# Kernel tuning notes

Hardware: AMD Instinct MI355X
Metric: run time of the kernel (lower is better)

Reference implementation:

```python
import jax, jax.numpy as jnp
import numpy as np

B, C, H = 16, 512, 32
HID, NB, S, P, SR = 512, 36, 26, 7, 2
SCALE = 32.0
N_LOC, N_LOC_LAB = 12, 8
N_GRP, GRP_SZ, N_GRP_LAB = 4, 6, 16
IN_DIM = P * P * C


def roi_align(feat, coords, scale, pooled, sr):
    # feat: (B,C,H,W); coords: (B,NB,4) normalized xyxy. torchvision roi_align,
    # aligned=False, fixed sampling_ratio=sr (adaptive ratio is data-dependent).
    Bs, Cc, Hh, Ww = feat.shape
    x1 = coords[..., 0] * scale
    y1 = coords[..., 1] * scale
    x2 = coords[..., 2] * scale
    y2 = coords[..., 3] * scale
    rw = jnp.maximum(x2 - x1, 1.0)
    rh = jnp.maximum(y2 - y1, 1.0)
    bw = rw / pooled
    bh = rh / pooled
    # sample offsets within roi, in bin units: (pooled*sr,)
    off = (jnp.arange(pooled)[:, None] + (jnp.arange(sr) + 0.5) / sr).reshape(-1)
    ys = y1[..., None] + off * bh[..., None]  # (B,NB,pooled*sr)
    xs = x1[..., None] + off * bw[..., None]

    def prep(t, size):
        valid = (t > -1.0) & (t < size)
        tc = jnp.clip(t, 0.0, size - 1)
        lo = jnp.floor(tc).astype(jnp.int32)
        hi = jnp.minimum(lo + 1, size - 1)
        frac = tc - lo
        return lo, hi, frac, valid

    y_lo, y_hi, ly, vy = prep(ys, Hh)
    x_lo, x_hi, lx, vx = prep(xs, Ww)
    hy, hx = 1.0 - ly, 1.0 - lx

    featl = feat.transpose(0, 2, 3, 1)  # (B,H,W,C)
    b_idx = jnp.arange(Bs)[:, None, None, None]

    def gather(yi, xi):
        # -> (B,NB,Py,Px,C)
        return featl[b_idx, yi[:, :, :, None], xi[:, :, None, :]]

    def w(a, b):
        return (a[..., :, None] * b[..., None, :])[..., None]

    val = (gather(y_lo, x_lo) * w(hy, hx) + gather(y_lo, x_hi) * w(hy, lx)
           + gather(y_hi, x_lo) * w(ly, hx) + gather(y_hi, x_hi) * w(ly, lx))
    mask = (vy[:, :, :, None] & vx[:, :, None, :])[..., None]
    val = jnp.where(mask, val, 0.0)
    val = val.reshape(Bs, -1, pooled, sr, pooled, sr, Cc).mean(axis=(3, 5))
    return val.transpose(0, 1, 4, 2, 3)  # (B,NB,C,pooled,pooled)


def setup_inputs() -> dict:
    key = jax.random.key(0)
    ks = jax.random.split(key, 10)
    lf = jax.random.normal(ks[0], (B, C, H, H), dtype=jnp.float32)
    xs = jnp.sort(jax.random.uniform(ks[1], (B, S, 2)), axis=-1)
    ys = jnp.sort(jax.random.uniform(ks[2], (B, S, 2)), axis=-1)
    coords = jnp.stack([xs[..., 0], ys[..., 0], xs[..., 1], ys[..., 1]], axis=-1)
    sc = 0.02
    return {
        'local_features': lf,
        'pred_bbox_coords': coords,
        'roi_fc_W': jax.random.normal(ks[3], (HID, IN_DIM), dtype=jnp.float32) * sc,
        'roi_fc_b': jnp.zeros((HID,), jnp.float32),
        'coords_W': jax.random.normal(ks[4], (S, 4, HID), dtype=jnp.float32) * sc,
        'coords_b': jnp.zeros((S, 4), jnp.float32),
        'pres_W': jax.random.normal(ks[5], (S, HID), dtype=jnp.float32) * sc,
        'pres_b': jnp.zeros((S,), jnp.float32),
        'loc_W': jax.random.normal(ks[6], (N_LOC, N_LOC_LAB, HID), dtype=jnp.float32) * sc,
        'loc_b': jnp.zeros((N_LOC, N_LOC_LAB), jnp.float32),
        'grp_W': jax.random.normal(ks[7], (N_GRP, N_GRP_LAB, GRP_SZ * HID), dtype=jnp.float32) * sc,
        'grp_b': jnp.zeros((N_GRP, N_GRP_LAB), jnp.float32),
        'loc_idx': jnp.arange(N_LOC, dtype=jnp.int32),
        'grp_idx': jnp.arange(N_GRP * GRP_SZ, dtype=jnp.int32).reshape(N_GRP, GRP_SZ),
    }


def reference(local_features, pred_bbox_coords, roi_fc_W, roi_fc_b, coords_W,
              coords_b, pres_W, pres_b, loc_W, loc_b, grp_W, grp_b, loc_idx, grp_idx):
    Bs = local_features.shape[0]
    # boxes S..NB default to the full image (0,0,1,1)
    full = jnp.broadcast_to(jnp.array([0.0, 0.0, 1.0, 1.0], jnp.float32), (Bs, NB, 4))
    coords_all = full.at[:, :S].set(pred_bbox_coords)
    roi = roi_align(local_features, coords_all, SCALE, P, SR)  # (B,NB,C,P,P)
    flat = roi.reshape(Bs, NB, IN_DIM)
    feats = jax.nn.relu(jnp.einsum('bnf,hf->bnh', flat, roi_fc_W) + roi_fc_b)
    sup = feats[:, :S]  # (B,S,HID)
    # per-box coord refinement heads
    deltas = jnp.einsum('bsh,soh->bso', sup, coords_W) + coords_b  # (B,S,4)
    w = pred_bbox_coords[..., 2] - pred_bbox_coords[..., 0]
    h = pred_bbox_coords[..., 3] - pred_bbox_coords[..., 1]
    wh = jnp.stack([w, h, w, h], axis=-1)
    refined = pred_bbox_coords + deltas * wh
    presence = jnp.einsum('bsh,sh->bs', sup, pres_W) + pres_b  # (B,S)
    # per-box MLC heads
    loc = jnp.einsum('blh,loh->blo', feats[:, loc_idx], loc_W) + loc_b
    # per-group MLC heads (concat box feats within group along hidden)
    gf = feats[:, grp_idx].reshape(Bs, N_GRP, GRP_SZ * HID)
    grp = jnp.einsum('bgk,gok->bgo', gf, grp_W) + grp_b
    mlc = jnp.concatenate([loc.reshape(Bs, -1), grp.reshape(Bs, -1)], axis=1)
    return refined, presence, mlc
```

## Files before the change

kernel.cpp:

```cpp
#include <hip/hip_runtime.h>

typedef unsigned short u16;
typedef __attribute__((ext_vector_type(8))) short short8;
typedef __attribute__((ext_vector_type(8))) unsigned short ushort8_t;
typedef __attribute__((ext_vector_type(4))) float f32x4;
typedef __attribute__((ext_vector_type(2))) float v2f;

#define BATCH   16
#define CCH     512
#define NBOX    36
#define SS      26
#define INDIM   25088
#define HIDN    512
#define M_ROWS  416
#define KSPLIT  56
#define KITERS  7
#define NKB     392

__device__ __forceinline__ u16 f2bf(float f) {
  unsigned u = __float_as_uint(f);
  u += 0x7FFF + ((u >> 16) & 1);
  return (u16)(u >> 16);
}
__device__ __forceinline__ float bf2f(u16 h) {
  return __uint_as_float(((unsigned)h) << 16);
}
__device__ __forceinline__ v2f bf2x2(u16 a, u16 b) {
  v2f r;
  r.x = __uint_as_float(((unsigned)a) << 16);
  r.y = __uint_as_float(((unsigned)b) << 16);
  return r;
}

__global__ __launch_bounds__(256) void k_transpose_lf(const float* __restrict__ in,
                                                      u16* __restrict__ out) {
  __shared__ u16 t[32][66];
  int b = blockIdx.z, y = blockIdx.y, ct = blockIdx.x;
  int tid = threadIdx.x;

  int cl = tid >> 2;
  int xq = (tid & 3) * 8;
  const float* src = in + ((size_t)(b * CCH + ct * 64 + cl) * 1024) + y * 32 + xq;
  float4 v0 = *(const float4*)src;
  float4 v1 = *(const float4*)(src + 4);
  t[xq + 0][cl] = f2bf(v0.x); t[xq + 1][cl] = f2bf(v0.y);
  t[xq + 2][cl] = f2bf(v0.z); t[xq + 3][cl] = f2bf(v0.w);
  t[xq + 4][cl] = f2bf(v1.x); t[xq + 5][cl] = f2bf(v1.y);
  t[xq + 6][cl] = f2bf(v1.z); t[xq + 7][cl] = f2bf(v1.w);
  __syncthreads();

  int xl = tid >> 3;
  int cq = (tid & 7) * 8;
  ushort8_t o;
#pragma unroll
  for (int i = 0; i < 8; ++i) o[i] = t[xl][cq + i];
  *(ushort8_t*)(out + ((size_t)b * 1024 + y * 32 + xl) * CCH + ct * 64 + cq) = o;
}

#define WPAD 532
__global__ __launch_bounds__(256) void k_convert_w(const float* __restrict__ in,
                                                   u16* __restrict__ out) {
  __shared__ u16 s[49 * WPAD];
  int h = blockIdx.x;
  int tid = threadIdx.x;
  const float4* src = (const float4*)(in + (size_t)h * INDIM);
  for (int i = tid; i < 6272; i += 256) {
    float4 v = src[i];
    int k = i * 4;
#pragma unroll
    for (int j = 0; j < 4; ++j) {
      int kk = k + j;
      int c = kk / 49;
      int p = kk - c * 49;
      s[p * WPAD + c] = f2bf((&v.x)[j]);
    }
  }
  __syncthreads();
  for (int q = tid; q < 3136; q += 256) {
    int p = q >> 6;
    int c0 = (q & 63) * 8;
    const u16* sp = &s[p * WPAD + c0];
    ushort8_t o;
#pragma unroll
    for (int i = 0; i < 8; ++i) o[i] = sp[i];
    int kb = p * 8 + (c0 >> 6);
    int col = c0 & 63;
    *(ushort8_t*)(out + ((size_t)kb * HIDN + h) * 64 + col) = o;
  }
}

__global__ __launch_bounds__(512) void k_roi(const u16* __restrict__ lf_t,
                                             const float* __restrict__ pred,
                                             u16* __restrict__ flat2) {
  __shared__ int   s_ylo[14], s_yhi[14], s_xlo[14], s_xhi[14];
  __shared__ float s_wyl[14], s_wyh[14], s_wxl[14], s_wxh[14];

  int bid = blockIdx.x;
  int xcd = bid & 7;
  int s = bid >> 3;
  int b = xcd * 2 + (s >= 26 ? 1 : 0);
  int n = (s >= 26) ? s - 26 : s;
  int blk = b * 26 + n;
  int t = threadIdx.x;

  if (t < 28) {
    bool isY = t < 14;
    int j = isY ? t : t - 14;
    const float* p = pred + ((size_t)(b * SS + n)) * 4;
    float c0 = p[0], c1 = p[1], c2 = p[2], c3 = p[3];
    float lo1 = (isY ? c1 : c0) * 32.f;
    float hi1 = (isY ? c3 : c2) * 32.f;
    float sz = fmaxf(hi1 - lo1, 1.f);
    float bs = sz * (1.f / 7.f);
    float off = (float)(j >> 1) + 0.25f + 0.5f * (float)(j & 1);
    float pos = lo1 + off * bs;
    bool valid = (pos > -1.f) && (pos < 32.f);
    float tc = fminf(fmaxf(pos, 0.f), 31.f);
    int lo = (int)floorf(tc);
    int hi = min(lo + 1, 31);
    float fr = tc - (float)lo;
    float wl = valid ? (1.f - fr) : 0.f;
    float wh = valid ? fr : 0.f;
    if (isY) { s_ylo[j] = lo; s_yhi[j] = hi; s_wyl[j] = wl; s_wyh[j] = wh; }
    else     { s_xlo[j] = lo; s_xhi[j] = hi; s_wxl[j] = wl; s_wxh[j] = wh; }
  }
  __syncthreads();

  int cg = t & 63;
  int pg = t >> 6;
  const u16* base = lf_t + (size_t)b * 1024 * CCH + cg * 8;

  for (int p = pg; p < 49; p += 8) {
    int py = p / 7, px = p % 7;
    v2f a0 = {0.f, 0.f}, a1 = {0.f, 0.f}, a2 = {0.f, 0.f}, a3 = {0.f, 0.f};
#pragma unroll
    for (int sy = 0; sy < 2; ++sy) {
      int jy = 2 * py + sy;
      const u16* rlo = base + s_ylo[jy] * 32 * CCH;
      const u16* rhi = base + s_yhi[jy] * 32 * CCH;
      float wyl = s_wyl[jy], wyh = s_wyh[jy];
#pragma unroll
      for (int sx = 0; sx < 2; ++sx) {
        int jx = 2 * px + sx;
        int xl = s_xlo[jx] * CCH, xh = s_xhi[jx] * CCH;
        v2f wll = {wyl * s_wxl[jx], wyl * s_wxl[jx]};
        v2f wlh = {wyl * s_wxh[jx], wyl * s_wxh[jx]};
        v2f whl = {wyh * s_wxl[jx], wyh * s_wxl[jx]};
        v2f whh = {wyh * s_wxh[jx], wyh * s_wxh[jx]};
        ushort8_t vll = *(const ushort8_t*)(rlo + xl);
        ushort8_t vlh = *(const ushort8_t*)(rlo + xh);
        ushort8_t vhl = *(const ushort8_t*)(rhi + xl);
        ushort8_t vhh = *(const ushort8_t*)(rhi + xh);
        a0 += wll * bf2x2(vll[0], vll[1]) + wlh * bf2x2(vlh[0], vlh[1])
            + whl * bf2x2(vhl[0], vhl[1]) + whh * bf2x2(vhh[0], vhh[1]);
        a1 += wll * bf2x2(vll[2], vll[3]) + wlh * bf2x2(vlh[2], vlh[3])
            + whl * bf2x2(vhl[2], vhl[3]) + whh * bf2x2(vhh[2], vhh[3]);
        a2 += wll * bf2x2(vll[4], vll[5]) + wlh * bf2x2(vlh[4], vlh[5])
            + whl * bf2x2(vhl[4], vhl[5]) + whh * bf2x2(vhh[4], vhh[5]);
        a3 += wll * bf2x2(vll[6], vll[7]) + wlh * bf2x2(vlh[6], vlh[7])
            + whl * bf2x2(vhl[6], vhl[7]) + whh * bf2x2(vhh[6], vhh[7]);
      }
    }
    ushort8_t o;
    o[0] = f2bf(a0.x * 0.25f); o[1] = f2bf(a0.y * 0.25f);
    o[2] = f2bf(a1.x * 0.25f); o[3] = f2bf(a1.y * 0.25f);
    o[4] = f2bf(a2.x * 0.25f); o[5] = f2bf(a2.y * 0.25f);
    o[6] = f2bf(a3.x * 0.25f); o[7] = f2bf(a3.y * 0.25f);
    int kb = p * 8 + (cg >> 3);
    int col = (cg & 7) * 8;
    *(ushort8_t*)(flat2 + ((size_t)kb * M_ROWS + blk) * 64 + col) = o;
  }
}

__global__ __launch_bounds__(256) void k_gemm(const u16* __restrict__ flat2,
                                              const u16* __restrict__ Wb2,
                                              u16* __restrict__ partials) {
  __shared__ u16 As[128 * 64];
  __shared__ u16 Bs[128 * 64];

  int tid = threadIdx.x;
  int wave = tid >> 6, lane = tid & 63;
  int wm = wave >> 1, wn = wave & 1;
  int quad = lane >> 4, r = lane & 15;
  int xb = r & 7;

  int bid = blockIdx.x;
  int xcd = bid & 7;
  int slot = bid >> 3;
  int z = xcd * 7 + (slot >> 4);
  int xy = slot & 15;
  int tileN0 = (xy & 3) * 128;
  int tileM0 = (xy >> 2) * 128;
  int kb0 = z * KITERS;

  size_t aoff[4], boff[4];
  int    ldso[4];
#pragma unroll
  for (int t = 0; t < 4; ++t) {
    int chunk = (wave * 4 + t) * 64 + lane;
    int row = chunk >> 3;
    int lc = chunk & 7;
    ldso[t] = row * 64 + ((lc ^ (row & 7)) << 3);
    int grow = min(tileM0 + row, M_ROWS - 1);
    aoff[t] = ((size_t)kb0 * M_ROWS + grow) * 64 + lc * 8;
    boff[t] = ((size_t)kb0 * HIDN + tileN0 + row) * 64 + lc * 8;
  }

  f32x4 acc[4][4];
#pragma unroll
  for (int mi = 0; mi < 4; ++mi)
#pragma unroll
    for (int ni = 0; ni < 4; ++ni) acc[mi][ni] = (f32x4){0.f, 0.f, 0.f, 0.f};

  short8 ra[4], rb[4];
#pragma unroll
  for (int t = 0; t < 4; ++t) {
    ra[t] = *(const short8*)(flat2 + aoff[t]);
    rb[t] = *(const short8*)(Wb2 + boff[t]);
  }

  for (int kt = 0; kt < KITERS; ++kt) {
#pragma unroll
    for (int t = 0; t < 4; ++t) {
      *(short8*)&As[ldso[t]] = ra[t];
      *(short8*)&Bs[ldso[t]] = rb[t];
    }
    __syncthreads();

    if (kt + 1 < KITERS) {
      size_t ak = (size_t)(kt + 1) * (M_ROWS * 64);
      size_t bk = (size_t)(kt + 1) * (HIDN * 64);
#pragma unroll
      for (int t = 0; t < 4; ++t) {
        ra[t] = *(const short8*)(flat2 + aoff[t] + ak);
        rb[t] = *(const short8*)(Wb2 + boff[t] + bk);
      }
    }

#pragma unroll
    for (int kk = 0; kk < 64; kk += 32) {
      int k8 = kk >> 3;
      int pc = ((k8 + quad) ^ xb) << 3;
      short8 af[4], bfr[4];
#pragma unroll
      for (int mi = 0; mi < 4; ++mi)
        af[mi] = *(const short8*)&As[(wm * 64 + mi * 16 + r) * 64 + pc];
#pragma unroll
      for (int ni = 0; ni < 4; ++ni)
        bfr[ni] = *(const short8*)&Bs[(wn * 64 + ni * 16 + r) * 64 + pc];
#pragma unroll
      for (int mi = 0; mi < 4; ++mi)
#pragma unroll
        for (int ni = 0; ni < 4; ++ni)
          acc[mi][ni] = __builtin_amdgcn_mfma_f32_16x16x32_bf16(
              af[mi], bfr[ni], acc[mi][ni], 0, 0, 0);
    }
    __syncthreads();
  }

  u16* part = partials + (size_t)z * (M_ROWS * HIDN);
#pragma unroll
  for (int mi = 0; mi < 4; ++mi)
#pragma unroll
    for (int ni = 0; ni < 4; ++ni) {
      int row0 = tileM0 + wm * 64 + mi * 16 + quad * 4;
      int col = tileN0 + wn * 64 + ni * 16 + r;
#pragma unroll
      for (int reg = 0; reg < 4; ++reg) {
        int row = row0 + reg;
        if (row < M_ROWS) part[(size_t)row * HIDN + col] = f2bf(acc[mi][ni][reg]);
      }
    }
}

__global__ __launch_bounds__(256) void k_reduce(const u16* __restrict__ partials,
                                                const float* __restrict__ bias,
                                                float* __restrict__ feats) {
  int gid = blockIdx.x * 256 + threadIdx.x;
  int row = gid >> 6;
  int c0 = (gid & 63) * 8;
  float s[8] = {0.f, 0.f, 0.f, 0.f, 0.f, 0.f, 0.f, 0.f};
  const u16* p = partials + (size_t)row * HIDN + c0;
  for (int z = 0; z < KSPLIT; ++z) {
    ushort8_t v = *(const ushort8_t*)(p + (size_t)z * (M_ROWS * HIDN));
#pragma unroll
    for (int j = 0; j < 8; ++j) s[j] += bf2f(v[j]);
  }
  float4 o0, o1;
  const float* bi = bias + c0;
  o0.x = fmaxf(s[0] + bi[0], 0.f); o0.y = fmaxf(s[1] + bi[1], 0.f);
  o0.z = fmaxf(s[2] + bi[2], 0.f); o0.w = fmaxf(s[3] + bi[3], 0.f);
  o1.x = fmaxf(s[4] + bi[4], 0.f); o1.y = fmaxf(s[5] + bi[5], 0.f);
  o1.z = fmaxf(s[6] + bi[6], 0.f); o1.w = fmaxf(s[7] + bi[7], 0.f);
  float* dst = feats + (size_t)row * HIDN + c0;
  *(float4*)dst = o0;
  *(float4*)(dst + 4) = o1;
}

__device__ __forceinline__ float wave_red(float s) {
#pragma unroll
  for (int off = 32; off > 0; off >>= 1) s += __shfl_down(s, off);
  return s;
}

__device__ __forceinline__ float dot512(const float* __restrict__ f,
                                        const float* __restrict__ w, int lane) {
  const float4* f4 = (const float4*)f;
  const float4* w4 = (const float4*)w;
  float4 x0 = f4[lane], y0 = w4[lane];
  float4 x1 = f4[lane + 64], y1 = w4[lane + 64];
  return x0.x * y0.x + x0.y * y0.y + x0.z * y0.z + x0.w * y0.w +
         x1.x * y1.x + x1.y * y1.y + x1.z * y1.z + x1.w * y1.w;
}

__global__ __launch_bounds__(256) void k_heads(const float* __restrict__ feats,
                                               const float* __restrict__ pred,
                                               const float* __restrict__ cW,
                                               const float* __restrict__ cb,
                                               const float* __restrict__ pW,
                                               const float* __restrict__ pb,
                                               const float* __restrict__ lW,
                                               const float* __restrict__ lb,
                                               const float* __restrict__ gW,
                                               const float* __restrict__ gb,
                                               const int* __restrict__ lidx,
                                               const int* __restrict__ gidx,
                                               float* __restrict__ out) {
  int wid = blockIdx.x * 4 + (threadIdx.x >> 6);
  int lane = threadIdx.x & 63;
  float sum = 0.f;

  if (wid < 1664) {
    int b = wid / 104, rr = wid % 104, s = rr >> 2, o = rr & 3;
    sum = dot512(feats + (size_t)(b * 26 + s) * HIDN,
                 cW + (size_t)(s * 4 + o) * HIDN, lane);
    sum = wave_red(sum);
    if (lane == 0) {
      const float* p = pred + (size_t)(b * SS + s) * 4;
      float wdt = p[2] - p[0], hgt = p[3] - p[1];
      float whv = (o & 1) ? hgt : wdt;
      out[wid] = p[o] + (sum + cb[s * 4 + o]) * whv;
    }
  } else if (wid < 2080) {
    int i = wid - 1664;
    int b = i / 26, s = i % 26;
    sum = dot512(feats + (size_t)(b * 26 + s) * HIDN,
                 pW + (size_t)s * HIDN, lane);
    sum = wave_red(sum);
    if (lane == 0) out[1664 + i] = sum + pb[s];
  } else if (wid < 3616) {
    int i = wid - 2080;
    int b = i / 96, rr = i % 96, l = rr >> 3, o = rr & 7;
    sum = dot512(feats + (size_t)(b * 26 + lidx[l]) * HIDN,
                 lW + (size_t)(l * 8 + o) * HIDN, lane);
    sum = wave_red(sum);
    if (lane == 0) out[2080 + b * 160 + rr] = sum + lb[l * 8 + o];
  } else {
    int i = wid - 3616;
    int b = i / 64, rr = i % 64, g = rr >> 4, o = rr & 15;
    const float* w = gW + (size_t)(g * 16 + o) * 3072;
#pragma unroll
    for (int jj = 0; jj < 6; ++jj) {
      sum += dot512(feats + (size_t)(b * 26 + gidx[g * 6 + jj]) * HIDN,
                    w + jj * 512, lane);
    }
    sum = wave_red(sum);
    if (lane == 0) out[2080 + b * 160 + 96 + rr] = sum + gb[g * 16 + o];
  }
}

extern "C" void kernel_launch(void* const* d_in, const int* in_sizes, int n_in,
                              void* d_out, int out_size, void* d_ws, size_t ws_size,
                              hipStream_t stream) {
  const float* lf      = (const float*)d_in[0];
  const float* pred    = (const float*)d_in[1];
  const float* roiW    = (const float*)d_in[2];
  const float* roiB    = (const float*)d_in[3];
  const float* cW      = (const float*)d_in[4];
  const float* cb      = (const float*)d_in[5];
  const float* pW      = (const float*)d_in[6];
  const float* pb      = (const float*)d_in[7];
  const float* lW      = (const float*)d_in[8];
  const float* lb      = (const float*)d_in[9];
  const float* gW      = (const float*)d_in[10];
  const float* gb      = (const float*)d_in[11];
  const int*   lidx    = (const int*)d_in[12];
  const int*   gidx    = (const int*)d_in[13];
  float* out = (float*)d_out;

  char* ws = (char*)d_ws;
  u16*   lf_t     = (u16*)ws;
  u16*   partials = (u16*)ws;
  u16*   Wb2   = (u16*)(ws + 33030144);
  u16*   flat2 = (u16*)(ws + 33030144 + 25690112);
  float* feats = (float*)(ws + 33030144 + 25690112 + 28901376);

  k_transpose_lf<<<dim3(8, 32, 16), 256, 0, stream>>>(lf, lf_t);
  k_convert_w<<<HIDN, 256, 0, stream>>>(roiW, Wb2);
  k_roi<<<M_ROWS, 512, 0, stream>>>(lf_t, pred, flat2);
  k_gemm<<<896, 256, 0, stream>>>(flat2, Wb2, partials);
  k_reduce<<<(M_ROWS * HIDN / 8) / 256, 256, 0, stream>>>(partials, roiB, feats);
  k_heads<<<1160, 256, 0, stream>>>(feats, pred, cW, cb, pW, pb, lW, lb, gW, gb,
                                    lidx, gidx, out);
}
```

Measured before the change: 203.2 us.

## Fuse all stages into one persistent kernel with software grid barriers

Merges the transpose, weight conversion, ROI align, split-K GEMM, reduction and head kernels into one persistent kernel of 256 blocks. The stages are separated by atomic-counter grid barriers, and a memset resets the counter before launch. This removes five kernel launches and the idle gaps between them. In exchange, several stages run on fewer blocks than before (256 instead of up to 4096), the barriers add spin-wait cost, and correctness relies on all 256 blocks being resident at once.

```diff
diff --git a/kernel.cpp b/kernel.cpp
--- a/kernel.cpp
+++ b/kernel.cpp
@@ -16,6 +16,7 @@
 #define KSPLIT  56
 #define KITERS  7
 #define NKB     392
+#define GRID    256
 
 __device__ __forceinline__ u16 f2bf(float f) {
   unsigned u = __float_as_uint(f);
@@ -32,269 +33,45 @@
   return r;
 }
 
-__global__ __launch_bounds__(256) void k_transpose_lf(const float* __restrict__ in,
-                                                      u16* __restrict__ out) {
-  __shared__ u16 t[32][66];
-  int b = blockIdx.z, y = blockIdx.y, ct = blockIdx.x;
-  int tid = threadIdx.x;
-
-  int cl = tid >> 2;
-  int xq = (tid & 3) * 8;
-  const float* src = in + ((size_t)(b * CCH + ct * 64 + cl) * 1024) + y * 32 + xq;
-  float4 v0 = *(const float4*)src;
-  float4 v1 = *(const float4*)(src + 4);
-  t[xq + 0][cl] = f2bf(v0.x); t[xq + 1][cl] = f2bf(v0.y);
-  t[xq + 2][cl] = f2bf(v0.z); t[xq + 3][cl] = f2bf(v0.w);
-  t[xq + 4][cl] = f2bf(v1.x); t[xq + 5][cl] = f2bf(v1.y);
-  t[xq + 6][cl] = f2bf(v1.z); t[xq + 7][cl] = f2bf(v1.w);
+struct KParams {
+  const float* lf;
+  const float* pred;
+  const float* roiW;
+  const float* roiB;
+  const float* cW;  const float* cb;
+  const float* pW;  const float* pb;
+  const float* lW;  const float* lb;
+  const float* gW;  const float* gb;
+  const int* lidx;  const int* gidx;
+  float* out;
+  u16* lf_t;
+  u16* Wb2;
+  u16* flat2;
+  u16* partials;
+  float* feats;
+  unsigned* bar;
+};
+
+union SMem {
+  u16 tr[32][66];
+  u16 cv[49 * 132];
+  struct { u16 A[128 * 64]; u16 B[128 * 64]; } g;
+  struct {
+    int   ylo[14], yhi[14], xlo[14], xhi[14];
+    float wyl[14], wyh[14], wxl[14], wxh[14];
+  } roi;
+};
+
+__device__ __forceinline__ void gbar(unsigned* ctr, unsigned target, int t) {
   __syncthreads();
-
-  int xl = tid >> 3;
-  int cq = (tid & 7) * 8;
-  ushort8_t o;
-#pragma unroll
-  for (int i = 0; i < 8; ++i) o[i] = t[xl][cq + i];
-  *(ushort8_t*)(out + ((size_t)b * 1024 + y * 32 + xl) * CCH + ct * 64 + cq) = o;
-}
-
-#define WPAD 532
-__global__ __launch_bounds__(256) void k_convert_w(const float* __restrict__ in,
-                                                   u16* __restrict__ out) {
-  __shared__ u16 s[49 * WPAD];
-  int h = blockIdx.x;
-  int tid = threadIdx.x;
-  const float4* src = (const float4*)(in + (size_t)h * INDIM);
-  for (int i = tid; i < 6272; i += 256) {
-    float4 v = src[i];
-    int k = i * 4;
-#pragma unroll
-    for (int j = 0; j < 4; ++j) {
-      int kk = k + j;
-      int c = kk / 49;
-      int p = kk - c * 49;
-      s[p * WPAD + c] = f2bf((&v.x)[j]);
-    }
+  if (t == 0) {
+    __threadfence();
+    __hip_atomic_fetch_add(ctr, 1u, __ATOMIC_ACQ_REL, __HIP_MEMORY_SCOPE_AGENT);
+    while (__hip_atomic_load(ctr, __ATOMIC_ACQUIRE, __HIP_MEMORY_SCOPE_AGENT) < target)
+      __builtin_amdgcn_s_sleep(2);
+    __threadfence();
   }
   __syncthreads();
-  for (int q = tid; q < 3136; q += 256) {
-    int p = q >> 6;
-    int c0 = (q & 63) * 8;
-    const u16* sp = &s[p * WPAD + c0];
-    ushort8_t o;
-#pragma unroll
-    for (int i = 0; i < 8; ++i) o[i] = sp[i];
-    int kb = p * 8 + (c0 >> 6);
-    int col = c0 & 63;
-    *(ushort8_t*)(out + ((size_t)kb * HIDN + h) * 64 + col) = o;
-  }
-}
-
-__global__ __launch_bounds__(512) void k_roi(const u16* __restrict__ lf_t,
-                                             const float* __restrict__ pred,
-                                             u16* __restrict__ flat2) {
-  __shared__ int   s_ylo[14], s_yhi[14], s_xlo[14], s_xhi[14];
-  __shared__ float s_wyl[14], s_wyh[14], s_wxl[14], s_wxh[14];
-
-  int bid = blockIdx.x;
-  int xcd = bid & 7;
-  int s = bid >> 3;
-  int b = xcd * 2 + (s >= 26 ? 1 : 0);
-  int n = (s >= 26) ? s - 26 : s;
-  int blk = b * 26 + n;
-  int t = threadIdx.x;
-
-  if (t < 28) {
-    bool isY = t < 14;
-    int j = isY ? t : t - 14;
-    const float* p = pred + ((size_t)(b * SS + n)) * 4;
-    float c0 = p[0], c1 = p[1], c2 = p[2], c3 = p[3];
-    float lo1 = (isY ? c1 : c0) * 32.f;
-    float hi1 = (isY ? c3 : c2) * 32.f;
-    float sz = fmaxf(hi1 - lo1, 1.f);
-    float bs = sz * (1.f / 7.f);
-    float off = (float)(j >> 1) + 0.25f + 0.5f * (float)(j & 1);
-    float pos = lo1 + off * bs;
-    bool valid = (pos > -1.f) && (pos < 32.f);
-    float tc = fminf(fmaxf(pos, 0.f), 31.f);
-    int lo = (int)floorf(tc);
-    int hi = min(lo + 1, 31);
-    float fr = tc - (float)lo;
-    float wl = valid ? (1.f - fr) : 0.f;
-    float wh = valid ? fr : 0.f;
-    if (isY) { s_ylo[j] = lo; s_yhi[j] = hi; s_wyl[j] = wl; s_wyh[j] = wh; }
-    else     { s_xlo[j] = lo; s_xhi[j] = hi; s_wxl[j] = wl; s_wxh[j] = wh; }
-  }
-  __syncthreads();
-
-  int cg = t & 63;
-  int pg = t >> 6;
-  const u16* base = lf_t + (size_t)b * 1024 * CCH + cg * 8;
-
-  for (int p = pg; p < 49; p += 8) {
-    int py = p / 7, px = p % 7;
-    v2f a0 = {0.f, 0.f}, a1 = {0.f, 0.f}, a2 = {0.f, 0.f}, a3 = {0.f, 0.f};
-#pragma unroll
-    for (int sy = 0; sy < 2; ++sy) {
-      int jy = 2 * py + sy;
-      const u16* rlo = base + s_ylo[jy] * 32 * CCH;
-      const u16* rhi = base + s_yhi[jy] * 32 * CCH;
-      float wyl = s_wyl[jy], wyh = s_wyh[jy];
-#pragma unroll
-      for (int sx = 0; sx < 2; ++sx) {
-        int jx = 2 * px + sx;
-        int xl = s_xlo[jx] * CCH, xh = s_xhi[jx] * CCH;
-        v2f wll = {wyl * s_wxl[jx], wyl * s_wxl[jx]};
-        v2f wlh = {wyl * s_wxh[jx], wyl * s_wxh[jx]};
-        v2f whl = {wyh * s_wxl[jx], wyh * s_wxl[jx]};
-        v2f whh = {wyh * s_wxh[jx], wyh * s_wxh[jx]};
-        ushort8_t vll = *(const ushort8_t*)(rlo + xl);
-        ushort8_t vlh = *(const ushort8_t*)(rlo + xh);
-        ushort8_t vhl = *(const ushort8_t*)(rhi + xl);
-        ushort8_t vhh = *(const ushort8_t*)(rhi + xh);
-        a0 += wll * bf2x2(vll[0], vll[1]) + wlh * bf2x2(vlh[0], vlh[1])
-            + whl * bf2x2(vhl[0], vhl[1]) + whh * bf2x2(vhh[0], vhh[1]);
-        a1 += wll * bf2x2(vll[2], vll[3]) + wlh * bf2x2(vlh[2], vlh[3])
-            + whl * bf2x2(vhl[2], vhl[3]) + whh * bf2x2(vhh[2], vhh[3]);
-        a2 += wll * bf2x2(vll[4], vll[5]) + wlh * bf2x2(vlh[4], vlh[5])
-            + whl * bf2x2(vhl[4], vhl[5]) + whh * bf2x2(vhh[4], vhh[5]);
-        a3 += wll * bf2x2(vll[6], vll[7]) + wlh * bf2x2(vlh[6], vlh[7])
-            + whl * bf2x2(vhl[6], vhl[7]) + whh * bf2x2(vhh[6], vhh[7]);
-      }
-    }
-    ushort8_t o;
-    o[0] = f2bf(a0.x * 0.25f); o[1] = f2bf(a0.y * 0.25f);
-    o[2] = f2bf(a1.x * 0.25f); o[3] = f2bf(a1.y * 0.25f);
-    o[4] = f2bf(a2.x * 0.25f); o[5] = f2bf(a2.y * 0.25f);
-    o[6] = f2bf(a3.x * 0.25f); o[7] = f2bf(a3.y * 0.25f);
-    int kb = p * 8 + (cg >> 3);
-    int col = (cg & 7) * 8;
-    *(ushort8_t*)(flat2 + ((size_t)kb * M_ROWS + blk) * 64 + col) = o;
-  }
-}
-
-__global__ __launch_bounds__(256) void k_gemm(const u16* __restrict__ flat2,
-                                              const u16* __restrict__ Wb2,
-                                              u16* __restrict__ partials) {
-  __shared__ u16 As[128 * 64];
-  __shared__ u16 Bs[128 * 64];
-
-  int tid = threadIdx.x;
-  int wave = tid >> 6, lane = tid & 63;
-  int wm = wave >> 1, wn = wave & 1;
-  int quad = lane >> 4, r = lane & 15;
-  int xb = r & 7;
-
-  int bid = blockIdx.x;
-  int xcd = bid & 7;
-  int slot = bid >> 3;
-  int z = xcd * 7 + (slot >> 4);
-  int xy = slot & 15;
-  int tileN0 = (xy & 3) * 128;
-  int tileM0 = (xy >> 2) * 128;
-  int kb0 = z * KITERS;
-
-  size_t aoff[4], boff[4];
-  int    ldso[4];
-#pragma unroll
-  for (int t = 0; t < 4; ++t) {
-    int chunk = (wave * 4 + t) * 64 + lane;
-    int row = chunk >> 3;
-    int lc = chunk & 7;
-    ldso[t] = row * 64 + ((lc ^ (row & 7)) << 3);
-    int grow = min(tileM0 + row, M_ROWS - 1);
-    aoff[t] = ((size_t)kb0 * M_ROWS + grow) * 64 + lc * 8;
-    boff[t] = ((size_t)kb0 * HIDN + tileN0 + row) * 64 + lc * 8;
-  }
-
-  f32x4 acc[4][4];
-#pragma unroll
-  for (int mi = 0; mi < 4; ++mi)
-#pragma unroll
-    for (int ni = 0; ni < 4; ++ni) acc[mi][ni] = (f32x4){0.f, 0.f, 0.f, 0.f};
-
-  short8 ra[4], rb[4];
-#pragma unroll
-  for (int t = 0; t < 4; ++t) {
-    ra[t] = *(const short8*)(flat2 + aoff[t]);
-    rb[t] = *(const short8*)(Wb2 + boff[t]);
-  }
-
-  for (int kt = 0; kt < KITERS; ++kt) {
-#pragma unroll
-    for (int t = 0; t < 4; ++t) {
-      *(short8*)&As[ldso[t]] = ra[t];
-      *(short8*)&Bs[ldso[t]] = rb[t];
-    }
-    __syncthreads();
-
-    if (kt + 1 < KITERS) {
-      size_t ak = (size_t)(kt + 1) * (M_ROWS * 64);
-      size_t bk = (size_t)(kt + 1) * (HIDN * 64);
-#pragma unroll
-      for (int t = 0; t < 4; ++t) {
-        ra[t] = *(const short8*)(flat2 + aoff[t] + ak);
-        rb[t] = *(const short8*)(Wb2 + boff[t] + bk);
-      }
-    }
-
-#pragma unroll
-    for (int kk = 0; kk < 64; kk += 32) {
-      int k8 = kk >> 3;
-      int pc = ((k8 + quad) ^ xb) << 3;
-      short8 af[4], bfr[4];
-#pragma unroll
-      for (int mi = 0; mi < 4; ++mi)
-        af[mi] = *(const short8*)&As[(wm * 64 + mi * 16 + r) * 64 + pc];
-#pragma unroll
-      for (int ni = 0; ni < 4; ++ni)
-        bfr[ni] = *(const short8*)&Bs[(wn * 64 + ni * 16 + r) * 64 + pc];
-#pragma unroll
-      for (int mi = 0; mi < 4; ++mi)
-#pragma unroll
-        for (int ni = 0; ni < 4; ++ni)
-          acc[mi][ni] = __builtin_amdgcn_mfma_f32_16x16x32_bf16(
-              af[mi], bfr[ni], acc[mi][ni], 0, 0, 0);
-    }
-    __syncthreads();
-  }
-
-  u16* part = partials + (size_t)z * (M_ROWS * HIDN);
-#pragma unroll
-  for (int mi = 0; mi < 4; ++mi)
-#pragma unroll
-    for (int ni = 0; ni < 4; ++ni) {
-      int row0 = tileM0 + wm * 64 + mi * 16 + quad * 4;
-      int col = tileN0 + wn * 64 + ni * 16 + r;
-#pragma unroll
-      for (int reg = 0; reg < 4; ++reg) {
-        int row = row0 + reg;
-        if (row < M_ROWS) part[(size_t)row * HIDN + col] = f2bf(acc[mi][ni][reg]);
-      }
-    }
-}
-
-__global__ __launch_bounds__(256) void k_reduce(const u16* __restrict__ partials,
-                                                const float* __restrict__ bias,
-                                                float* __restrict__ feats) {
-  int gid = blockIdx.x * 256 + threadIdx.x;
-  int row = gid >> 6;
-  int c0 = (gid & 63) * 8;
-  float s[8] = {0.f, 0.f, 0.f, 0.f, 0.f, 0.f, 0.f, 0.f};
-  const u16* p = partials + (size_t)row * HIDN + c0;
-  for (int z = 0; z < KSPLIT; ++z) {
-    ushort8_t v = *(const ushort8_t*)(p + (size_t)z * (M_ROWS * HIDN));
-#pragma unroll
-    for (int j = 0; j < 8; ++j) s[j] += bf2f(v[j]);
-  }
-  float4 o0, o1;
-  const float* bi = bias + c0;
-  o0.x = fmaxf(s[0] + bi[0], 0.f); o0.y = fmaxf(s[1] + bi[1], 0.f);
-  o0.z = fmaxf(s[2] + bi[2], 0.f); o0.w = fmaxf(s[3] + bi[3], 0.f);
-  o1.x = fmaxf(s[4] + bi[4], 0.f); o1.y = fmaxf(s[5] + bi[5], 0.f);
-  o1.z = fmaxf(s[6] + bi[6], 0.f); o1.w = fmaxf(s[7] + bi[7], 0.f);
-  float* dst = feats + (size_t)row * HIDN + c0;
-  *(float4*)dst = o0;
-  *(float4*)(dst + 4) = o1;
 }
 
 __device__ __forceinline__ float wave_red(float s) {
@@ -313,93 +90,337 @@
          x1.x * y1.x + x1.y * y1.y + x1.z * y1.z + x1.w * y1.w;
 }
 
-__global__ __launch_bounds__(256) void k_heads(const float* __restrict__ feats,
-                                               const float* __restrict__ pred,
-                                               const float* __restrict__ cW,
-                                               const float* __restrict__ cb,
-                                               const float* __restrict__ pW,
-                                               const float* __restrict__ pb,
-                                               const float* __restrict__ lW,
-                                               const float* __restrict__ lb,
-                                               const float* __restrict__ gW,
-                                               const float* __restrict__ gb,
-                                               const int* __restrict__ lidx,
-                                               const int* __restrict__ gidx,
-                                               float* __restrict__ out) {
-  int wid = blockIdx.x * 4 + (threadIdx.x >> 6);
-  int lane = threadIdx.x & 63;
-  float sum = 0.f;
-
-  if (wid < 1664) {
-    int b = wid / 104, rr = wid % 104, s = rr >> 2, o = rr & 3;
-    sum = dot512(feats + (size_t)(b * 26 + s) * HIDN,
-                 cW + (size_t)(s * 4 + o) * HIDN, lane);
-    sum = wave_red(sum);
-    if (lane == 0) {
-      const float* p = pred + (size_t)(b * SS + s) * 4;
-      float wdt = p[2] - p[0], hgt = p[3] - p[1];
-      float whv = (o & 1) ? hgt : wdt;
-      out[wid] = p[o] + (sum + cb[s * 4 + o]) * whv;
-    }
-  } else if (wid < 2080) {
-    int i = wid - 1664;
-    int b = i / 26, s = i % 26;
-    sum = dot512(feats + (size_t)(b * 26 + s) * HIDN,
-                 pW + (size_t)s * HIDN, lane);
-    sum = wave_red(sum);
-    if (lane == 0) out[1664 + i] = sum + pb[s];
-  } else if (wid < 3616) {
-    int i = wid - 2080;
-    int b = i / 96, rr = i % 96, l = rr >> 3, o = rr & 7;
-    sum = dot512(feats + (size_t)(b * 26 + lidx[l]) * HIDN,
-                 lW + (size_t)(l * 8 + o) * HIDN, lane);
-    sum = wave_red(sum);
-    if (lane == 0) out[2080 + b * 160 + rr] = sum + lb[l * 8 + o];
-  } else {
-    int i = wid - 3616;
-    int b = i / 64, rr = i % 64, g = rr >> 4, o = rr & 15;
-    const float* w = gW + (size_t)(g * 16 + o) * 3072;
-#pragma unroll
-    for (int jj = 0; jj < 6; ++jj) {
-      sum += dot512(feats + (size_t)(b * 26 + gidx[g * 6 + jj]) * HIDN,
-                    w + jj * 512, lane);
-    }
-    sum = wave_red(sum);
-    if (lane == 0) out[2080 + b * 160 + 96 + rr] = sum + gb[g * 16 + o];
+__global__ __launch_bounds__(256, 2) void k_fused(KParams P) {
+  __shared__ SMem sm;
+  const int t   = threadIdx.x;
+  const int bid = blockIdx.x;
+
+  for (int j = bid; j < 6144; j += GRID) {
+    if (j < 4096) {
+      int ct = j & 7, y = (j >> 3) & 31, b = j >> 8;
+      int cl = t >> 2;
+      int xq = (t & 3) * 8;
+      const float* src = P.lf + ((size_t)(b * CCH + ct * 64 + cl) * 1024) + y * 32 + xq;
+      float4 v0 = *(const float4*)src;
+      float4 v1 = *(const float4*)(src + 4);
+      sm.tr[xq + 0][cl] = f2bf(v0.x); sm.tr[xq + 1][cl] = f2bf(v0.y);
+      sm.tr[xq + 2][cl] = f2bf(v0.z); sm.tr[xq + 3][cl] = f2bf(v0.w);
+      sm.tr[xq + 4][cl] = f2bf(v1.x); sm.tr[xq + 5][cl] = f2bf(v1.y);
+      sm.tr[xq + 6][cl] = f2bf(v1.z); sm.tr[xq + 7][cl] = f2bf(v1.w);
+      __syncthreads();
+      int xl = t >> 3;
+      int cq = (t & 7) * 8;
+      ushort8_t o;
+#pragma unroll
+      for (int i = 0; i < 8; ++i) o[i] = sm.tr[xl][cq + i];
+      *(ushort8_t*)(P.lf_t + ((size_t)b * 1024 + y * 32 + xl) * CCH + ct * 64 + cq) = o;
+    } else {
+      int j2 = j - 4096;
+      int h  = j2 >> 2;
+      int c0 = (j2 & 3) * 128;
+      const float4* s4 = (const float4*)(P.roiW + (size_t)h * INDIM + (size_t)c0 * 49);
+      for (int i = t; i < 1568; i += 256) {
+        float4 v = s4[i];
+        int k = i * 4;
+#pragma unroll
+        for (int jj = 0; jj < 4; ++jj) {
+          int kk = k + jj;
+          int cc = kk / 49;
+          int p  = kk - cc * 49;
+          sm.cv[p * 132 + cc] = f2bf((&v.x)[jj]);
+        }
+      }
+      __syncthreads();
+      for (int q = t; q < 784; q += 256) {
+        int p = q >> 4;
+        int cc0 = (q & 15) * 8;
+        const u16* sp = &sm.cv[p * 132 + cc0];
+        ushort8_t o;
+#pragma unroll
+        for (int i = 0; i < 8; ++i) o[i] = sp[i];
+        int c   = c0 + cc0;
+        int kb  = p * 8 + (c >> 6);
+        int col = c & 63;
+        *(ushort8_t*)(P.Wb2 + ((size_t)kb * HIDN + h) * 64 + col) = o;
+      }
+    }
+    __syncthreads();
+  }
+  gbar(P.bar, 1 * GRID, t);
+
+  for (int j = bid; j < 832; j += GRID) {
+    int half = (j >= 416) ? 1 : 0;
+    int bj   = half ? j - 416 : j;
+    int xcd  = bj & 7;
+    int s    = bj >> 3;
+    int b    = xcd * 2 + (s >= 26 ? 1 : 0);
+    int n    = (s >= 26) ? s - 26 : s;
+    int blk  = b * 26 + n;
+
+    if (t < 28) {
+      bool isY = t < 14;
+      int jj = isY ? t : t - 14;
+      const float* pp = P.pred + ((size_t)(b * SS + n)) * 4;
+      float c0 = pp[0], c1 = pp[1], c2 = pp[2], c3 = pp[3];
+      float lo1 = (isY ? c1 : c0) * 32.f;
+      float hi1 = (isY ? c3 : c2) * 32.f;
+      float sz = fmaxf(hi1 - lo1, 1.f);
+      float bs = sz * (1.f / 7.f);
+      float off = (float)(jj >> 1) + 0.25f + 0.5f * (float)(jj & 1);
+      float pos = lo1 + off * bs;
+      bool valid = (pos > -1.f) && (pos < 32.f);
+      float tc = fminf(fmaxf(pos, 0.f), 31.f);
+      int lo = (int)floorf(tc);
+      int hi = min(lo + 1, 31);
+      float fr = tc - (float)lo;
+      float wl = valid ? (1.f - fr) : 0.f;
+      float wh = valid ? fr : 0.f;
+      if (isY) { sm.roi.ylo[jj] = lo; sm.roi.yhi[jj] = hi;
+                 sm.roi.wyl[jj] = wl; sm.roi.wyh[jj] = wh; }
+      else     { sm.roi.xlo[jj] = lo; sm.roi.xhi[jj] = hi;
+                 sm.roi.wxl[jj] = wl; sm.roi.wxh[jj] = wh; }
+    }
+    __syncthreads();
+
+    int cgi = t & 63;
+    int pg  = t >> 6;
+    const u16* base = P.lf_t + (size_t)b * 1024 * CCH + cgi * 8;
+    int pend = half ? 49 : 24;
+
+    for (int p = (half ? 24 : 0) + pg; p < pend; p += 4) {
+      int py = p / 7, px = p % 7;
+      v2f a0 = {0.f, 0.f}, a1 = {0.f, 0.f}, a2 = {0.f, 0.f}, a3 = {0.f, 0.f};
+#pragma unroll
+      for (int sy = 0; sy < 2; ++sy) {
+        int jy = 2 * py + sy;
+        const u16* rlo = base + sm.roi.ylo[jy] * 32 * CCH;
+        const u16* rhi = base + sm.roi.yhi[jy] * 32 * CCH;
+        float wyl = sm.roi.wyl[jy], wyh = sm.roi.wyh[jy];
+#pragma unroll
+        for (int sx = 0; sx < 2; ++sx) {
+          int jx = 2 * px + sx;
+          int xl = sm.roi.xlo[jx] * CCH, xh = sm.roi.xhi[jx] * CCH;
+          v2f wll = {wyl * sm.roi.wxl[jx], wyl * sm.roi.wxl[jx]};
+          v2f wlh = {wyl * sm.roi.wxh[jx], wyl * sm.roi.wxh[jx]};
+          v2f whl = {wyh * sm.roi.wxl[jx], wyh * sm.roi.wxl[jx]};
+          v2f whh = {wyh * sm.roi.wxh[jx], wyh * sm.roi.wxh[jx]};
+          ushort8_t vll = *(const ushort8_t*)(rlo + xl);
+          ushort8_t vlh = *(const ushort8_t*)(rlo + xh);
+          ushort8_t vhl = *(const ushort8_t*)(rhi + xl);
+          ushort8_t vhh = *(const ushort8_t*)(rhi + xh);
+          a0 += wll * bf2x2(vll[0], vll[1]) + wlh * bf2x2(vlh[0], vlh[1])
+              + whl * bf2x2(vhl[0], vhl[1]) + whh * bf2x2(vhh[0], vhh[1]);
+          a1 += wll * bf2x2(vll[2], vll[3]) + wlh * bf2x2(vlh[2], vlh[3])
+              + whl * bf2x2(vhl[2], vhl[3]) + whh * bf2x2(vhh[2], vhh[3]);
+          a2 += wll * bf2x2(vll[4], vll[5]) + wlh * bf2x2(vlh[4], vlh[5])
+              + whl * bf2x2(vhl[4], vhl[5]) + whh * bf2x2(vhh[4], vhh[5]);
+          a3 += wll * bf2x2(vll[6], vll[7]) + wlh * bf2x2(vlh[6], vlh[7])
+              + whl * bf2x2(vhl[6], vhl[7]) + whh * bf2x2(vhh[6], vhh[7]);
+        }
+      }
+      ushort8_t o;
+      o[0] = f2bf(a0.x * 0.25f); o[1] = f2bf(a0.y * 0.25f);
+      o[2] = f2bf(a1.x * 0.25f); o[3] = f2bf(a1.y * 0.25f);
+      o[4] = f2bf(a2.x * 0.25f); o[5] = f2bf(a2.y * 0.25f);
+      o[6] = f2bf(a3.x * 0.25f); o[7] = f2bf(a3.y * 0.25f);
+      int kb  = p * 8 + (cgi >> 3);
+      int col = (cgi & 7) * 8;
+      *(ushort8_t*)(P.flat2 + ((size_t)kb * M_ROWS + blk) * 64 + col) = o;
+    }
+    __syncthreads();
+  }
+  gbar(P.bar, 2 * GRID, t);
+
+  for (int job = bid; job < 896; job += GRID) {
+    int wave = t >> 6, lane = t & 63;
+    int wm = wave >> 1, wn = wave & 1;
+    int quad = lane >> 4, r = lane & 15;
+    int xb = r & 7;
+
+    int xcd2 = job & 7;
+    int slot = job >> 3;
+    int z  = xcd2 * 7 + (slot >> 4);
+    int xy = slot & 15;
+    int tileN0 = (xy & 3) * 128;
+    int tileM0 = (xy >> 2) * 128;
+    int kb0 = z * KITERS;
+
+    size_t aoff[4], boff[4];
+    int    ldso[4];
+#pragma unroll
+    for (int tt = 0; tt < 4; ++tt) {
+      int chunk = (wave * 4 + tt) * 64 + lane;
+      int row = chunk >> 3;
+      int lc  = chunk & 7;
+      ldso[tt] = row * 64 + ((lc ^ (row & 7)) << 3);
+      int grow = min(tileM0 + row, M_ROWS - 1);
+      aoff[tt] = ((size_t)kb0 * M_ROWS + grow) * 64 + lc * 8;
+      boff[tt] = ((size_t)kb0 * HIDN + tileN0 + row) * 64 + lc * 8;
+    }
+
+    f32x4 acc[4][4];
+#pragma unroll
+    for (int mi = 0; mi < 4; ++mi)
+#pragma unroll
+      for (int ni = 0; ni < 4; ++ni) acc[mi][ni] = (f32x4){0.f, 0.f, 0.f, 0.f};
+
+    short8 ra[4], rb[4];
+#pragma unroll
+    for (int tt = 0; tt < 4; ++tt) {
+      ra[tt] = *(const short8*)(P.flat2 + aoff[tt]);
+      rb[tt] = *(const short8*)(P.Wb2 + boff[tt]);
+    }
+
+    for (int kt = 0; kt < KITERS; ++kt) {
+#pragma unroll
+      for (int tt = 0; tt < 4; ++tt) {
+        *(short8*)&sm.g.A[ldso[tt]] = ra[tt];
+        *(short8*)&sm.g.B[ldso[tt]] = rb[tt];
+      }
+      __syncthreads();
+
+      if (kt + 1 < KITERS) {
+        size_t ak = (size_t)(kt + 1) * (M_ROWS * 64);
+        size_t bk = (size_t)(kt + 1) * (HIDN * 64);
+#pragma unroll
+        for (int tt = 0; tt < 4; ++tt) {
+          ra[tt] = *(const short8*)(P.flat2 + aoff[tt] + ak);
+          rb[tt] = *(const short8*)(P.Wb2 + boff[tt] + bk);
+        }
+      }
+
+#pragma unroll
+      for (int kk = 0; kk < 64; kk += 32) {
+        int k8 = kk >> 3;
+        int pc = ((k8 + quad) ^ xb) << 3;
+        short8 af[4], bfr[4];
+#pragma unroll
+        for (int mi = 0; mi < 4; ++mi)
+          af[mi] = *(const short8*)&sm.g.A[(wm * 64 + mi * 16 + r) * 64 + pc];
+#pragma unroll
+        for (int ni = 0; ni < 4; ++ni)
+          bfr[ni] = *(const short8*)&sm.g.B[(wn * 64 + ni * 16 + r) * 64 + pc];
+#pragma unroll
+        for (int mi = 0; mi < 4; ++mi)
+#pragma unroll
+          for (int ni = 0; ni < 4; ++ni)
+            acc[mi][ni] = __builtin_amdgcn_mfma_f32_16x16x32_bf16(
+                af[mi], bfr[ni], acc[mi][ni], 0, 0, 0);
+      }
+      __syncthreads();
+    }
+
+    u16* part = P.partials + (size_t)z * (M_ROWS * HIDN);
+#pragma unroll
+    for (int mi = 0; mi < 4; ++mi)
+#pragma unroll
+      for (int ni = 0; ni < 4; ++ni) {
+        int row0 = tileM0 + wm * 64 + mi * 16 + quad * 4;
+        int col  = tileN0 + wn * 64 + ni * 16 + r;
+#pragma unroll
+        for (int reg = 0; reg < 4; ++reg) {
+          int row = row0 + reg;
+          if (row < M_ROWS) part[(size_t)row * HIDN + col] = f2bf(acc[mi][ni][reg]);
+        }
+      }
+  }
+  gbar(P.bar, 3 * GRID, t);
+
+  for (int gid = bid * 256 + t; gid < M_ROWS * HIDN / 8; gid += GRID * 256) {
+    int row = gid >> 6;
+    int c0  = (gid & 63) * 8;
+    float s[8] = {0.f, 0.f, 0.f, 0.f, 0.f, 0.f, 0.f, 0.f};
+    const u16* p = P.partials + (size_t)row * HIDN + c0;
+    for (int z = 0; z < KSPLIT; ++z) {
+      ushort8_t v = *(const ushort8_t*)(p + (size_t)z * (M_ROWS * HIDN));
+#pragma unroll
+      for (int jj = 0; jj < 8; ++jj) s[jj] += bf2f(v[jj]);
+    }
+    float4 o0, o1;
+    const float* bi = P.roiB + c0;
+    o0.x = fmaxf(s[0] + bi[0], 0.f); o0.y = fmaxf(s[1] + bi[1], 0.f);
+    o0.z = fmaxf(s[2] + bi[2], 0.f); o0.w = fmaxf(s[3] + bi[3], 0.f);
+    o1.x = fmaxf(s[4] + bi[4], 0.f); o1.y = fmaxf(s[5] + bi[5], 0.f);
+    o1.z = fmaxf(s[6] + bi[6], 0.f); o1.w = fmaxf(s[7] + bi[7], 0.f);
+    float* dst = P.feats + (size_t)row * HIDN + c0;
+    *(float4*)dst = o0;
+    *(float4*)(dst + 4) = o1;
+  }
+  gbar(P.bar, 4 * GRID, t);
+
+  for (int j = bid; j < 1160; j += GRID) {
+    int wid  = j * 4 + (t >> 6);
+    int lane = t & 63;
+    float sum = 0.f;
+
+    if (wid < 1664) {
+      int b = wid / 104, rr = wid % 104, s = rr >> 2, o = rr & 3;
+      sum = dot512(P.feats + (size_t)(b * 26 + s) * HIDN,
+                   P.cW + (size_t)(s * 4 + o) * HIDN, lane);
+      sum = wave_red(sum);
+      if (lane == 0) {
+        const float* pp = P.pred + (size_t)(b * SS + s) * 4;
+        float wdt = pp[2] - pp[0], hgt = pp[3] - pp[1];
+        float whv = (o & 1) ? hgt : wdt;
+        P.out[wid] = pp[o] + (sum + P.cb[s * 4 + o]) * whv;
+      }
+    } else if (wid < 2080) {
+      int i = wid - 1664;
+      int b = i / 26, s = i % 26;
+      sum = dot512(P.feats + (size_t)(b * 26 + s) * HIDN,
+                   P.pW + (size_t)s * HIDN, lane);
+      sum = wave_red(sum);
+      if (lane == 0) P.out[1664 + i] = sum + P.pb[s];
+    } else if (wid < 3616) {
+      int i = wid - 2080;
+      int b = i / 96, rr = i % 96, l = rr >> 3, o = rr & 7;
+      sum = dot512(P.feats + (size_t)(b * 26 + P.lidx[l]) * HIDN,
+                   P.lW + (size_t)(l * 8 + o) * HIDN, lane);
+      sum = wave_red(sum);
+      if (lane == 0) P.out[2080 + b * 160 + rr] = sum + P.lb[l * 8 + o];
+    } else {
+      int i = wid - 3616;
+      int b = i / 64, rr = i % 64, g = rr >> 4, o = rr & 15;
+      const float* w = P.gW + (size_t)(g * 16 + o) * 3072;
+#pragma unroll
+      for (int jj = 0; jj < 6; ++jj) {
+        sum += dot512(P.feats + (size_t)(b * 26 + P.gidx[g * 6 + jj]) * HIDN,
+                      w + jj * 512, lane);
+      }
+      sum = wave_red(sum);
+      if (lane == 0) P.out[2080 + b * 160 + 96 + rr] = sum + P.gb[g * 16 + o];
+    }
   }
 }
 
 extern "C" void kernel_launch(void* const* d_in, const int* in_sizes, int n_in,
                               void* d_out, int out_size, void* d_ws, size_t ws_size,
                               hipStream_t stream) {
-  const float* lf      = (const float*)d_in[0];
-  const float* pred    = (const float*)d_in[1];
-  const float* roiW    = (const float*)d_in[2];
-  const float* roiB    = (const float*)d_in[3];
-  const float* cW      = (const float*)d_in[4];
-  const float* cb      = (const float*)d_in[5];
-  const float* pW      = (const float*)d_in[6];
-  const float* pb      = (const float*)d_in[7];
-  const float* lW      = (const float*)d_in[8];
-  const float* lb      = (const float*)d_in[9];
-  const float* gW      = (const float*)d_in[10];
-  const float* gb      = (const float*)d_in[11];
-  const int*   lidx    = (const int*)d_in[12];
-  const int*   gidx    = (const int*)d_in[13];
-  float* out = (float*)d_out;
-
   char* ws = (char*)d_ws;
-  u16*   lf_t     = (u16*)ws;
-  u16*   partials = (u16*)ws;
-  u16*   Wb2   = (u16*)(ws + 33030144);
-  u16*   flat2 = (u16*)(ws + 33030144 + 25690112);
-  float* feats = (float*)(ws + 33030144 + 25690112 + 28901376);
-
-  k_transpose_lf<<<dim3(8, 32, 16), 256, 0, stream>>>(lf, lf_t);
-  k_convert_w<<<HIDN, 256, 0, stream>>>(roiW, Wb2);
-  k_roi<<<M_ROWS, 512, 0, stream>>>(lf_t, pred, flat2);
-  k_gemm<<<896, 256, 0, stream>>>(flat2, Wb2, partials);
-  k_reduce<<<(M_ROWS * HIDN / 8) / 256, 256, 0, stream>>>(partials, roiB, feats);
-  k_heads<<<1160, 256, 0, stream>>>(feats, pred, cW, cb, pW, pb, lW, lb, gW, gb,
-                                    lidx, gidx, out);
-}
+
+  KParams hp;
+  hp.lf    = (const float*)d_in[0];
+  hp.pred  = (const float*)d_in[1];
+  hp.roiW  = (const float*)d_in[2];
+  hp.roiB  = (const float*)d_in[3];
+  hp.cW    = (const float*)d_in[4];
+  hp.cb    = (const float*)d_in[5];
+  hp.pW    = (const float*)d_in[6];
+  hp.pb    = (const float*)d_in[7];
+  hp.lW    = (const float*)d_in[8];
+  hp.lb    = (const float*)d_in[9];
+  hp.gW    = (const float*)d_in[10];
+  hp.gb    = (const float*)d_in[11];
+  hp.lidx  = (const int*)d_in[12];
+  hp.gidx  = (const int*)d_in[13];
+  hp.out   = (float*)d_out;
+  hp.lf_t     = (u16*)ws;
+  hp.partials = (u16*)ws;
+  hp.Wb2      = (u16*)(ws + 33030144);
+  hp.flat2    = (u16*)(ws + 33030144 + 25690112);
+  hp.bar      = (unsigned*)(ws + 33030144 + 25690112 + 20873216);
+  hp.feats    = (float*)(ws + 33030144 + 25690112 + 28901376);
+
+  hipMemsetAsync((void*)hp.bar, 0, 64, stream);
+  k_fused<<<dim3(GRID), dim3(256), 0, stream>>>(hp);
+}
```

Measured after the change: 434.7 us. 114% more time.

## Merge preprocessing kernels and split weight conversion and reduction across more threads

Applied to the files above, without the earlier changes.

Fuses the feature transpose and weight conversion into one launch. The weight conversion is split from 512 blocks of one hidden row each into 2048 blocks, each handling a quarter of the channels, so each block uses less shared memory and occupancy is higher. The split-K reduction now has two threads per output vector, each summing half the partials, combined with a shuffle, which doubles parallelism in the reduce. This saves a launch and relieves the under-parallelised weight conversion, at the cost of branch divergence between block roles.

```diff
diff --git a/kernel.cpp b/kernel.cpp
--- a/kernel.cpp
+++ b/kernel.cpp
@@ -32,60 +32,64 @@
   return r;
 }
 
-__global__ __launch_bounds__(256) void k_transpose_lf(const float* __restrict__ in,
-                                                      u16* __restrict__ out) {
-  __shared__ u16 t[32][66];
-  int b = blockIdx.z, y = blockIdx.y, ct = blockIdx.x;
-  int tid = threadIdx.x;
-
-  int cl = tid >> 2;
-  int xq = (tid & 3) * 8;
-  const float* src = in + ((size_t)(b * CCH + ct * 64 + cl) * 1024) + y * 32 + xq;
-  float4 v0 = *(const float4*)src;
-  float4 v1 = *(const float4*)(src + 4);
-  t[xq + 0][cl] = f2bf(v0.x); t[xq + 1][cl] = f2bf(v0.y);
-  t[xq + 2][cl] = f2bf(v0.z); t[xq + 3][cl] = f2bf(v0.w);
-  t[xq + 4][cl] = f2bf(v1.x); t[xq + 5][cl] = f2bf(v1.y);
-  t[xq + 6][cl] = f2bf(v1.z); t[xq + 7][cl] = f2bf(v1.w);
-  __syncthreads();
-
-  int xl = tid >> 3;
-  int cq = (tid & 7) * 8;
-  ushort8_t o;
-#pragma unroll
-  for (int i = 0; i < 8; ++i) o[i] = t[xl][cq + i];
-  *(ushort8_t*)(out + ((size_t)b * 1024 + y * 32 + xl) * CCH + ct * 64 + cq) = o;
-}
-
-#define WPAD 532
-__global__ __launch_bounds__(256) void k_convert_w(const float* __restrict__ in,
-                                                   u16* __restrict__ out) {
-  __shared__ u16 s[49 * WPAD];
-  int h = blockIdx.x;
-  int tid = threadIdx.x;
-  const float4* src = (const float4*)(in + (size_t)h * INDIM);
-  for (int i = tid; i < 6272; i += 256) {
-    float4 v = src[i];
-    int k = i * 4;
-#pragma unroll
-    for (int j = 0; j < 4; ++j) {
-      int kk = k + j;
-      int c = kk / 49;
-      int p = kk - c * 49;
-      s[p * WPAD + c] = f2bf((&v.x)[j]);
-    }
-  }
-  __syncthreads();
-  for (int q = tid; q < 3136; q += 256) {
-    int p = q >> 6;
-    int c0 = (q & 63) * 8;
-    const u16* sp = &s[p * WPAD + c0];
+__global__ __launch_bounds__(256) void k_prep(const float* __restrict__ lf,
+                                              const float* __restrict__ roiW,
+                                              u16* __restrict__ lf_t,
+                                              u16* __restrict__ Wb2) {
+  __shared__ union {
+    u16 tr[32][66];
+    u16 cv[49 * 132];
+  } sm;
+  int j = blockIdx.x;
+  int t = threadIdx.x;
+
+  if (j < 4096) {
+    int ct = j & 7, y = (j >> 3) & 31, b = j >> 8;
+    int cl = t >> 2;
+    int xq = (t & 3) * 8;
+    const float* src = lf + ((size_t)(b * CCH + ct * 64 + cl) * 1024) + y * 32 + xq;
+    float4 v0 = *(const float4*)src;
+    float4 v1 = *(const float4*)(src + 4);
+    sm.tr[xq + 0][cl] = f2bf(v0.x); sm.tr[xq + 1][cl] = f2bf(v0.y);
+    sm.tr[xq + 2][cl] = f2bf(v0.z); sm.tr[xq + 3][cl] = f2bf(v0.w);
+    sm.tr[xq + 4][cl] = f2bf(v1.x); sm.tr[xq + 5][cl] = f2bf(v1.y);
+    sm.tr[xq + 6][cl] = f2bf(v1.z); sm.tr[xq + 7][cl] = f2bf(v1.w);
+    __syncthreads();
+    int xl = t >> 3;
+    int cq = (t & 7) * 8;
     ushort8_t o;
 #pragma unroll
-    for (int i = 0; i < 8; ++i) o[i] = sp[i];
-    int kb = p * 8 + (c0 >> 6);
-    int col = c0 & 63;
-    *(ushort8_t*)(out + ((size_t)kb * HIDN + h) * 64 + col) = o;
+    for (int i = 0; i < 8; ++i) o[i] = sm.tr[xl][cq + i];
+    *(ushort8_t*)(lf_t + ((size_t)b * 1024 + y * 32 + xl) * CCH + ct * 64 + cq) = o;
+  } else {
+    int j2 = j - 4096;
+    int h  = j2 >> 2;
+    int c0 = (j2 & 3) * 128;
+    const float4* s4 = (const float4*)(roiW + (size_t)h * INDIM + (size_t)c0 * 49);
+    for (int i = t; i < 1568; i += 256) {
+      float4 v = s4[i];
+      int k = i * 4;
+#pragma unroll
+      for (int jj = 0; jj < 4; ++jj) {
+        int kk = k + jj;
+        int cc = kk / 49;
+        int p  = kk - cc * 49;
+        sm.cv[p * 132 + cc] = f2bf((&v.x)[jj]);
+      }
+    }
+    __syncthreads();
+    for (int q = t; q < 784; q += 256) {
+      int p = q >> 4;
+      int cc0 = (q & 15) * 8;
+      const u16* sp = &sm.cv[p * 132 + cc0];
+      ushort8_t o;
+#pragma unroll
+      for (int i = 0; i < 8; ++i) o[i] = sp[i];
+      int c   = c0 + cc0;
+      int kb  = p * 8 + (c >> 6);
+      int col = c & 63;
+      *(ushort8_t*)(Wb2 + ((size_t)kb * HIDN + h) * 64 + col) = o;
+    }
   }
 }
 
@@ -277,24 +281,31 @@
                                                 const float* __restrict__ bias,
                                                 float* __restrict__ feats) {
   int gid = blockIdx.x * 256 + threadIdx.x;
-  int row = gid >> 6;
-  int c0 = (gid & 63) * 8;
+  int zh  = gid & 1;
+  int idx = gid >> 1;
+  int row = idx >> 6;
+  int c0  = (idx & 63) * 8;
   float s[8] = {0.f, 0.f, 0.f, 0.f, 0.f, 0.f, 0.f, 0.f};
-  const u16* p = partials + (size_t)row * HIDN + c0;
-  for (int z = 0; z < KSPLIT; ++z) {
+  const u16* p = partials + (size_t)row * HIDN + c0
+               + (size_t)(zh * 28) * (M_ROWS * HIDN);
+  for (int z = 0; z < 28; ++z) {
     ushort8_t v = *(const ushort8_t*)(p + (size_t)z * (M_ROWS * HIDN));
 #pragma unroll
     for (int j = 0; j < 8; ++j) s[j] += bf2f(v[j]);
   }
-  float4 o0, o1;
-  const float* bi = bias + c0;
-  o0.x = fmaxf(s[0] + bi[0], 0.f); o0.y = fmaxf(s[1] + bi[1], 0.f);
-  o0.z = fmaxf(s[2] + bi[2], 0.f); o0.w = fmaxf(s[3] + bi[3], 0.f);
-  o1.x = fmaxf(s[4] + bi[4], 0.f); o1.y = fmaxf(s[5] + bi[5], 0.f);
-  o1.z = fmaxf(s[6] + bi[6], 0.f); o1.w = fmaxf(s[7] + bi[7], 0.f);
-  float* dst = feats + (size_t)row * HIDN + c0;
-  *(float4*)dst = o0;
-  *(float4*)(dst + 4) = o1;
+#pragma unroll
+  for (int j = 0; j < 8; ++j) s[j] += __shfl_xor(s[j], 1);
+  if (zh == 0) {
+    float4 o0, o1;
+    const float* bi = bias + c0;
+    o0.x = fmaxf(s[0] + bi[0], 0.f); o0.y = fmaxf(s[1] + bi[1], 0.f);
+    o0.z = fmaxf(s[2] + bi[2], 0.f); o0.w = fmaxf(s[3] + bi[3], 0.f);
+    o1.x = fmaxf(s[4] + bi[4], 0.f); o1.y = fmaxf(s[5] + bi[5], 0.f);
+    o1.z = fmaxf(s[6] + bi[6], 0.f); o1.w = fmaxf(s[7] + bi[7], 0.f);
+    float* dst = feats + (size_t)row * HIDN + c0;
+    *(float4*)dst = o0;
+    *(float4*)(dst + 4) = o1;
+  }
 }
 
 __device__ __forceinline__ float wave_red(float s) {
@@ -395,11 +406,10 @@
   u16*   flat2 = (u16*)(ws + 33030144 + 25690112);
   float* feats = (float*)(ws + 33030144 + 25690112 + 28901376);
 
-  k_transpose_lf<<<dim3(8, 32, 16), 256, 0, stream>>>(lf, lf_t);
-  k_convert_w<<<HIDN, 256, 0, stream>>>(roiW, Wb2);
+  k_prep<<<6144, 256, 0, stream>>>(lf, roiW, lf_t, Wb2);
   k_roi<<<M_ROWS, 512, 0, stream>>>(lf_t, pred, flat2);
   k_gemm<<<896, 256, 0, stream>>>(flat2, Wb2, partials);
-  k_reduce<<<(M_ROWS * HIDN / 8) / 256, 256, 0, stream>>>(partials, roiB, feats);
+  k_reduce<<<208, 256, 0, stream>>>(partials, roiB, feats);
   k_heads<<<1160, 256, 0, stream>>>(feats, pred, cW, cb, pW, pb, lW, lb, gW, gb,
                                     lidx, gidx, out);
 }
```

Result: faster. 192.4 us, median of 2 (-5.3%).
